# Optimization experiments

Measured on AMD Instinct MI355X. Metric: run time of the kernel, lower is better.

The kernel has to match this reference:

```python
import jax, jax.numpy as jnp
import numpy as np

B, N, C, H = 16, 1029, 1024, 16
D = C // H  # head_dim = 64
N_ROPE = 1024  # patch tokens covered by rope; prefix = N - N_ROPE = 5


def setup_inputs() -> dict:
    key = jax.random.key(0)
    ks = jax.random.split(key, 8)
    x = jax.random.normal(ks[0], (B, N, C), dtype=jnp.float32)
    rope_sin = jax.random.uniform(ks[1], (N_ROPE, D), dtype=jnp.float32, minval=-1.0, maxval=1.0)
    rope_cos = jax.random.uniform(ks[2], (N_ROPE, D), dtype=jnp.float32, minval=-1.0, maxval=1.0)
    s = 1.0 / np.sqrt(C)
    W_qkv = jax.random.normal(ks[3], (3 * C, C), dtype=jnp.float32) * s
    b_qkv = jax.random.normal(ks[4], (3 * C,), dtype=jnp.float32) * 0.02
    W_proj = jax.random.normal(ks[5], (C, C), dtype=jnp.float32) * s
    b_proj = jax.random.normal(ks[6], (C,), dtype=jnp.float32) * 0.02
    return {"x": x, "rope_sin": rope_sin, "rope_cos": rope_cos,
            "W_qkv": W_qkv, "b_qkv": b_qkv, "W_proj": W_proj, "b_proj": b_proj}


def _rotate_half(t):
    t1, t2 = jnp.split(t, 2, axis=-1)
    return jnp.concatenate([-t2, t1], axis=-1)


def _rope_apply(t, sin, cos):
    # t: [B, H, N_rope, D]; sin/cos: [N_rope, D] broadcast over B, H
    return t * cos + _rotate_half(t) * sin


def reference(x, rope_sin, rope_cos, W_qkv, b_qkv, W_proj, b_proj):
    b, n, c = x.shape
    h, d = H, c // H
    # QKV projection (torch Linear: x @ W.T + b)
    qkv = x @ W_qkv.T + b_qkv                       # [B, N, 3C]
    qkv = qkv.reshape(b, n, 3, h, d)
    q = jnp.transpose(qkv[:, :, 0], (0, 2, 1, 3))   # [B, H, N, D]
    k = jnp.transpose(qkv[:, :, 1], (0, 2, 1, 3))
    v = jnp.transpose(qkv[:, :, 2], (0, 2, 1, 3))
    # RoPE on the patch-token suffix only
    prefix = n - rope_sin.shape[-2]
    q = jnp.concatenate([q[:, :, :prefix], _rope_apply(q[:, :, prefix:], rope_sin, rope_cos)], axis=2)
    k = jnp.concatenate([k[:, :, :prefix], _rope_apply(k[:, :, prefix:], rope_sin, rope_cos)], axis=2)
    # Scaled dot-product attention (default scale = 1/sqrt(D))
    scale = 1.0 / jnp.sqrt(jnp.asarray(d, dtype=x.dtype))
    scores = jnp.einsum('bhqd,bhkd->bhqk', q, k) * scale
    attn = jax.nn.softmax(scores, axis=-1)
    out = jnp.einsum('bhqk,bhkd->bhqd', attn, v)    # [B, H, N, D]
    out = jnp.transpose(out, (0, 2, 1, 3)).reshape(b, n, c)
    # Output projection
    return out @ W_proj.T + b_proj
```

## Files before the change

kernel.cpp:

```cpp
#include <hip/hip_runtime.h>
#include <cfloat>
#include <math.h>

#define B_      16
#define N_TOK   1029
#define C_      1024
#define H_      16
#define D_      64
#define PREFIX  5
#define M_ROWS  (B_ * N_TOK)
#define HEAD_SLAB ((size_t)B_ * H_ * N_TOK * D_)
#define VT_STRIDE 1088

typedef __attribute__((ext_vector_type(8))) short bf16x8;
typedef __attribute__((ext_vector_type(4))) float f32x4;

__device__ __forceinline__ unsigned short f2bf(float f) {
    unsigned u = __float_as_uint(f);
    u += 0x7fffu + ((u >> 16) & 1u);
    return (unsigned short)(u >> 16);
}
__device__ __forceinline__ float bf2f(unsigned short h) {
    return __uint_as_float(((unsigned)h) << 16);
}

__global__ __launch_bounds__(256)
void split_kernel(const float* __restrict__ in, unsigned short* __restrict__ hi,
                  unsigned short* __restrict__ lo, int n4)
{
    const int i = blockIdx.x * 256 + threadIdx.x;
    if (i >= n4) return;
    const float4 v = ((const float4*)in)[i];
    ushort4 h, l;
    h.x = f2bf(v.x); l.x = f2bf(v.x - bf2f(h.x));
    h.y = f2bf(v.y); l.y = f2bf(v.y - bf2f(h.y));
    h.z = f2bf(v.z); l.z = f2bf(v.z - bf2f(h.z));
    h.w = f2bf(v.w); l.w = f2bf(v.w - bf2f(h.w));
    ((ushort4*)hi)[i] = h;
    ((ushort4*)lo)[i] = l;
}

__device__ __forceinline__ bf16x8 frag_ld(const unsigned short* slab, int r, int q) {
    const int L = r >> 1;
    const int s = (q | ((r & 1) << 2)) ^ (L & 7);
    return *(const bf16x8*)(slab + L * 64 + s * 8);
}

#define WAIT_BAR(N) do {                                          \
    asm volatile("s_waitcnt vmcnt(" #N ")" ::: "memory");         \
    __builtin_amdgcn_s_barrier();                                 \
    __builtin_amdgcn_sched_barrier(0);                            \
} while (0)

__global__ __launch_bounds__(512, 2)
void gemm_mfma8(const unsigned short* __restrict__ Ahi, const unsigned short* __restrict__ Alo,
                const unsigned short* __restrict__ Whi, const unsigned short* __restrict__ Wlo,
                const float* __restrict__ bias, float* __restrict__ out,
                int M, int Ncols, int K, int scatter)
{
    __shared__ unsigned short lds[2][4][256 * 32];

    const int tid  = threadIdx.x;
    const int wave = tid >> 6;
    const int lane = tid & 63;
    const int lm   = lane & 15;
    const int quad = lane >> 4;
    const int bx = blockIdx.x, by = blockIdx.y;
    const int wm = wave >> 2;
    const int wn = wave & 3;
    const int rowA = by * 256;
    const int rowB = bx * 256;

    f32x4 acc[8][4];
#pragma unroll
    for (int mi = 0; mi < 8; ++mi)
#pragma unroll
        for (int ni = 0; ni < 4; ++ni)
            acc[mi][ni] = (f32x4){0.f, 0.f, 0.f, 0.f};

#define STAGE(buf_, slab_, base_, row0_, doClamp_, k0_) do {                          \
    _Pragma("unroll")                                                                 \
    for (int i_ = 0; i_ < 2; ++i_) {                                                  \
        const int c_ = i_ * 512 + tid;                                                \
        const int L_ = c_ >> 3;                                                       \
        const int u_ = (c_ & 7) ^ (L_ & 7);                                           \
        int grow_ = (row0_) + 2 * L_ + (u_ >> 2);                                     \
        if (doClamp_) grow_ = min(grow_, M - 1);                                      \
        const unsigned short* src_ = (base_) + (size_t)grow_ * K + (k0_) + (u_ & 3) * 8; \
        __builtin_amdgcn_global_load_lds(                                             \
            (__attribute__((address_space(1))) void*)src_,                            \
            (__attribute__((address_space(3))) void*)&lds[buf_][slab_][(i_ * 512 + wave * 64) * 8], \
            16, 0, 0);                                                                \
    }                                                                                 \
} while (0)

    STAGE(0, 0, Ahi, rowA, true,  0);
    STAGE(0, 2, Whi, rowB, false, 0);
    STAGE(0, 3, Wlo, rowB, false, 0);
    STAGE(0, 1, Alo, rowA, true,  0);

    const int NT = K >> 5;
    for (int t = 0; t < NT; ++t) {
        const int cur = t & 1, nxt = cur ^ 1;
        const int tn = (t + 1 == NT) ? 0 : t + 1;
        const int k1 = tn << 5;

        WAIT_BAR(4);
        STAGE(nxt, 0, Ahi, rowA, true,  k1);
        STAGE(nxt, 2, Whi, rowB, false, k1);
        bf16x8 b[4], a[8];
#pragma unroll
        for (int ni = 0; ni < 4; ++ni)
            b[ni] = frag_ld(&lds[cur][2][0], wn * 64 + ni * 16 + lm, quad);
#pragma unroll
        for (int mi = 0; mi < 8; ++mi)
            a[mi] = frag_ld(&lds[cur][0][0], wm * 128 + mi * 16 + lm, quad);
        __builtin_amdgcn_s_setprio(1);
#pragma unroll
        for (int mi = 0; mi < 8; ++mi)
#pragma unroll
            for (int ni = 0; ni < 4; ++ni)
                acc[mi][ni] = __builtin_amdgcn_mfma_f32_16x16x32_bf16(a[mi], b[ni], acc[mi][ni], 0, 0, 0);
        __builtin_amdgcn_s_setprio(0);

        WAIT_BAR(6);
        STAGE(nxt, 3, Wlo, rowB, false, k1);
        __builtin_amdgcn_s_setprio(1);
#pragma unroll
        for (int ni = 0; ni < 4; ++ni) {
            const bf16x8 bl = frag_ld(&lds[cur][3][0], wn * 64 + ni * 16 + lm, quad);
#pragma unroll
            for (int mi = 0; mi < 8; ++mi)
                acc[mi][ni] = __builtin_amdgcn_mfma_f32_16x16x32_bf16(a[mi], bl, acc[mi][ni], 0, 0, 0);
        }
        __builtin_amdgcn_s_setprio(0);

        WAIT_BAR(6);
        STAGE(nxt, 1, Alo, rowA, true, k1);
        __builtin_amdgcn_s_setprio(1);
#pragma unroll
        for (int mi = 0; mi < 8; ++mi) {
            const bf16x8 al = frag_ld(&lds[cur][1][0], wm * 128 + mi * 16 + lm, quad);
#pragma unroll
            for (int ni = 0; ni < 4; ++ni)
                acc[mi][ni] = __builtin_amdgcn_mfma_f32_16x16x32_bf16(al, b[ni], acc[mi][ni], 0, 0, 0);
        }
        __builtin_amdgcn_s_setprio(0);
    }
#undef STAGE
    asm volatile("s_waitcnt vmcnt(0)" ::: "memory");

#pragma unroll
    for (int mi = 0; mi < 8; ++mi) {
#pragma unroll
        for (int rr = 0; rr < 4; ++rr) {
            const int gm = rowA + wm * 128 + mi * 16 + quad * 4 + rr;
            if (gm >= M) continue;
            if (!scatter) {
#pragma unroll
                for (int ni = 0; ni < 4; ++ni) {
                    const int gn = rowB + wn * 64 + ni * 16 + lm;
                    out[(size_t)gm * Ncols + gn] = acc[mi][ni][rr] + bias[gn];
                }
            } else {
                const int b_  = gm / N_TOK;
                const int tok = gm - b_ * N_TOK;
#pragma unroll
                for (int ni = 0; ni < 4; ++ni) {
                    const int gn    = rowB + wn * 64 + ni * 16 + lm;
                    const int which = gn >> 10;
                    const int h     = (gn >> 6) & 15;
                    const int d     = gn & 63;
                    const size_t dst = (size_t)which * HEAD_SLAB +
                                       (((size_t)(b_ * H_ + h)) * N_TOK + tok) * 64 + d;
                    out[dst] = acc[mi][ni][rr] + bias[gn];
                }
            }
        }
    }
}
#undef WAIT_BAR

__global__ __launch_bounds__(256)
void rope_convert(const float* __restrict__ qf, const float* __restrict__ kf,
                  const float* __restrict__ sin_, const float* __restrict__ cos_,
                  unsigned short* __restrict__ qhi, unsigned short* __restrict__ qlo,
                  unsigned short* __restrict__ khi, unsigned short* __restrict__ klo)
{
    const int idx = blockIdx.x * 256 + threadIdx.x;
    const int total = B_ * H_ * N_TOK * 32;
    if (idx >= total) return;
    const int d   = idx & 31;
    const int tmp = idx >> 5;
    const int n   = tmp % N_TOK;
    const int bh  = tmp / N_TOK;

    const size_t base = ((size_t)bh * N_TOK + n) * 64;
    float q1 = qf[base + d], q2 = qf[base + d + 32];
    float k1 = kf[base + d], k2 = kf[base + d + 32];

    if (n >= PREFIX) {
        const int r = n - PREFIX;
        const float c1 = cos_[r * 64 + d];
        const float c2 = cos_[r * 64 + d + 32];
        const float s1 = sin_[r * 64 + d];
        const float s2 = sin_[r * 64 + d + 32];
        const float nq1 = q1 * c1 - q2 * s1;
        const float nq2 = q2 * c2 + q1 * s2;
        q1 = nq1; q2 = nq2;
        const float nk1 = k1 * c1 - k2 * s1;
        const float nk2 = k2 * c2 + k1 * s2;
        k1 = nk1; k2 = nk2;
    }
    q1 *= 0.125f; q2 *= 0.125f;

    unsigned short h;
    h = f2bf(q1); qhi[base + d]      = h; qlo[base + d]      = f2bf(q1 - bf2f(h));
    h = f2bf(q2); qhi[base + d + 32] = h; qlo[base + d + 32] = f2bf(q2 - bf2f(h));
    h = f2bf(k1); khi[base + d]      = h; klo[base + d]      = f2bf(k1 - bf2f(h));
    h = f2bf(k2); khi[base + d + 32] = h; klo[base + d + 32] = f2bf(k2 - bf2f(h));
}

__global__ __launch_bounds__(256)
void v_transpose(const float* __restrict__ vf, unsigned short* __restrict__ vt)
{
    __shared__ float t[64][65];
    const int tid = threadIdx.x;
    const int kt0 = blockIdx.x * 64;
    const int bh  = blockIdx.y;
    const float* src = vf + (size_t)bh * N_TOK * 64;

#pragma unroll
    for (int p = 0; p < 4; ++p) {
        const int e   = p * 256 + tid;
        const int key = e >> 4;
        const int c4  = (e & 15) << 2;
        const int gk  = kt0 + key;
        float4 v = make_float4(0.f, 0.f, 0.f, 0.f);
        if (gk < N_TOK) v = *(const float4*)(src + (size_t)gk * 64 + c4);
        t[key][c4 + 0] = v.x;
        t[key][c4 + 1] = v.y;
        t[key][c4 + 2] = v.z;
        t[key][c4 + 3] = v.w;
    }
    __syncthreads();

    const int d  = tid >> 2;
    const int kb = (tid & 3) << 4;
    unsigned short buf[16];
#pragma unroll
    for (int j = 0; j < 16; ++j) buf[j] = f2bf(t[kb + j][d]);
    unsigned short* dst = vt + (size_t)bh * 64 * VT_STRIDE + (size_t)d * VT_STRIDE + kt0 + kb;
#pragma unroll
    for (int j = 0; j < 4; ++j)
        *(ushort4*)(dst + j * 4) = *(ushort4*)&buf[j * 4];
}

__global__ __launch_bounds__(512, 4)
void attn_mfma2(const unsigned short* __restrict__ qhi_g, const unsigned short* __restrict__ qlo_g,
                const unsigned short* __restrict__ khi_g, const unsigned short* __restrict__ klo_g,
                const unsigned short* __restrict__ vt_g,
                unsigned short* __restrict__ Ohi, unsigned short* __restrict__ Olo)
{
    __shared__ unsigned short Khl[2][64 * 64];
    __shared__ unsigned short Kll[2][64 * 64];
    __shared__ unsigned short Vtl[2][64 * 64];
    __shared__ unsigned short Pl[128 * 64];

    const int tid  = threadIdx.x;
    const int wave = tid >> 6;
    const int lane = tid & 63;
    const int lm   = lane & 15;
    const int quad = lane >> 4;
    const int bh   = blockIdx.x;
    const int q0   = blockIdx.y * 128;
    const int b    = bh >> 4;
    const int h    = bh & 15;

    const unsigned short* Qh  = qhi_g + (size_t)bh * N_TOK * 64;
    const unsigned short* Ql  = qlo_g + (size_t)bh * N_TOK * 64;
    const unsigned short* Khb = khi_g + (size_t)bh * N_TOK * 64;
    const unsigned short* Klb = klo_g + (size_t)bh * N_TOK * 64;
    const unsigned short* Vtb = vt_g  + (size_t)bh * 64 * VT_STRIDE;

#define STAGE(bs, kt0_) do {                                                     \
    const int r_  = tid >> 3;                                                    \
    const int qs_ = tid & 7;                                                     \
    const int sw_ = (qs_ ^ (r_ & 7)) << 3;                                       \
    const int ldsoff_ = wave * 512;                                              \
    const int gk_ = min((kt0_) + r_, N_TOK - 1);                                 \
    __builtin_amdgcn_global_load_lds(                                            \
        (__attribute__((address_space(1))) void*)(Khb + (size_t)gk_ * 64 + sw_), \
        (__attribute__((address_space(3))) void*)&Khl[bs][ldsoff_], 16, 0, 0);   \
    __builtin_amdgcn_global_load_lds(                                            \
        (__attribute__((address_space(1))) void*)(Klb + (size_t)gk_ * 64 + sw_), \
        (__attribute__((address_space(3))) void*)&Kll[bs][ldsoff_], 16, 0, 0);   \
    __builtin_amdgcn_global_load_lds(                                            \
        (__attribute__((address_space(1))) void*)(Vtb + (size_t)r_ * VT_STRIDE + (kt0_) + sw_), \
        (__attribute__((address_space(3))) void*)&Vtl[bs][ldsoff_], 16, 0, 0);   \
} while (0)

    STAGE(0, 0);

    bf16x8 qh[2], ql[2];
    {
        int row = q0 + wave * 16 + lm;
        if (row > N_TOK - 1) row = N_TOK - 1;
#pragma unroll
        for (int s = 0; s < 2; ++s) {
            const size_t off = (size_t)row * 64 + s * 32 + quad * 8;
            qh[s] = *(const bf16x8*)&Qh[off];
            ql[s] = *(const bf16x8*)&Ql[off];
        }
    }

    f32x4 o[4];
    float m_i[4], l_i[4];
#pragma unroll
    for (int r = 0; r < 4; ++r) {
        m_i[r] = -FLT_MAX;
        l_i[r] = 0.f;
        o[r] = (f32x4){0.f, 0.f, 0.f, 0.f};
    }

    asm volatile("s_waitcnt vmcnt(0)\n\ts_barrier" ::: "memory");

    for (int kt = 0; kt < 17; ++kt) {
        const int kt0 = kt * 64;
        const int cur = kt & 1;

        if (kt < 16) STAGE(cur ^ 1, kt0 + 64);

        f32x4 s_acc[4];
#pragma unroll
        for (int ct = 0; ct < 4; ++ct)
            s_acc[ct] = (f32x4){0.f, 0.f, 0.f, 0.f};

#pragma unroll
        for (int ct = 0; ct < 4; ++ct) {
            const int krow = ct * 16 + lm;
#pragma unroll
            for (int s = 0; s < 2; ++s) {
                const int chunk = ((s * 4 + quad) ^ (krow & 7)) << 3;
                const bf16x8 kbh = *(const bf16x8*)&Khl[cur][krow * 64 + chunk];
                const bf16x8 kbl = *(const bf16x8*)&Kll[cur][krow * 64 + chunk];
                s_acc[ct] = __builtin_amdgcn_mfma_f32_16x16x32_bf16(qh[s], kbh, s_acc[ct], 0, 0, 0);
                s_acc[ct] = __builtin_amdgcn_mfma_f32_16x16x32_bf16(qh[s], kbl, s_acc[ct], 0, 0, 0);
                s_acc[ct] = __builtin_amdgcn_mfma_f32_16x16x32_bf16(ql[s], kbh, s_acc[ct], 0, 0, 0);
            }
        }

        if (kt0 + 64 > N_TOK) {
#pragma unroll
            for (int ct = 0; ct < 4; ++ct) {
                if (kt0 + ct * 16 + lm >= N_TOK) {
#pragma unroll
                    for (int r = 0; r < 4; ++r) s_acc[ct][r] = -FLT_MAX;
                }
            }
        }

#pragma unroll
        for (int r = 0; r < 4; ++r) {
            float mt = fmaxf(fmaxf(s_acc[0][r], s_acc[1][r]),
                             fmaxf(s_acc[2][r], s_acc[3][r]));
            mt = fmaxf(mt, __shfl_xor(mt, 1));
            mt = fmaxf(mt, __shfl_xor(mt, 2));
            mt = fmaxf(mt, __shfl_xor(mt, 4));
            mt = fmaxf(mt, __shfl_xor(mt, 8));
            const float mnew  = fmaxf(m_i[r], mt);
            const float alpha = __expf(m_i[r] - mnew);
            float pv[4], rs = 0.f;
#pragma unroll
            for (int ct = 0; ct < 4; ++ct) {
                pv[ct] = __expf(s_acc[ct][r] - mnew);
                rs += pv[ct];
            }
            rs += __shfl_xor(rs, 1);
            rs += __shfl_xor(rs, 2);
            rs += __shfl_xor(rs, 4);
            rs += __shfl_xor(rs, 8);
            l_i[r] = l_i[r] * alpha + rs;
            m_i[r] = mnew;
#pragma unroll
            for (int dt = 0; dt < 4; ++dt) o[dt][r] *= alpha;
            const int prow = wave * 16 + quad * 4 + r;
#pragma unroll
            for (int ct = 0; ct < 4; ++ct) {
                const int col = ct * 16 + lm;
                const int idx = prow * 64 + ((((col >> 3) ^ (prow & 7)) << 3) | (col & 7));
                Pl[idx] = f2bf(pv[ct]);
            }
        }

#pragma unroll
        for (int ks = 0; ks < 2; ++ks) {
            const int prow = wave * 16 + lm;
            const int chunk = ((ks * 4 + quad) ^ (prow & 7)) << 3;
            const bf16x8 pf = *(const bf16x8*)&Pl[prow * 64 + chunk];
#pragma unroll
            for (int dt = 0; dt < 4; ++dt) {
                const int vrow = dt * 16 + lm;
                const int chunkv = ((ks * 4 + quad) ^ (vrow & 7)) << 3;
                const bf16x8 vh = *(const bf16x8*)&Vtl[cur][vrow * 64 + chunkv];
                o[dt] = __builtin_amdgcn_mfma_f32_16x16x32_bf16(pf, vh, o[dt], 0, 0, 0);
            }
        }

        asm volatile("s_waitcnt vmcnt(0)\n\ts_barrier" ::: "memory");
    }
#undef STAGE

#pragma unroll
    for (int r = 0; r < 4; ++r) {
        const int gq = q0 + wave * 16 + quad * 4 + r;
        if (gq >= N_TOK) continue;
        const float inv = 1.0f / l_i[r];
        const size_t base = (((size_t)(b * N_TOK + gq)) * H_ + h) * D_;
#pragma unroll
        for (int dt = 0; dt < 4; ++dt) {
            const float val = o[dt][r] * inv;
            const unsigned short hb = f2bf(val);
            Ohi[base + dt * 16 + lm] = hb;
            Olo[base + dt * 16 + lm] = f2bf(val - bf2f(hb));
        }
    }
}

extern "C" void kernel_launch(void* const* d_in, const int* in_sizes, int n_in,
                              void* d_out, int out_size, void* d_ws, size_t ws_size,
                              hipStream_t stream)
{
    const float* x        = (const float*)d_in[0];
    const float* rope_sin = (const float*)d_in[1];
    const float* rope_cos = (const float*)d_in[2];
    const float* W_qkv    = (const float*)d_in[3];
    const float* b_qkv    = (const float*)d_in[4];
    const float* W_proj   = (const float*)d_in[5];
    const float* b_proj   = (const float*)d_in[6];
    float* out = (float*)d_out;

    float* q_buf = (float*)d_ws;
    float* k_buf = q_buf + HEAD_SLAB;
    float* v_buf = q_buf + 2 * HEAD_SLAB;
    float* slab4 = q_buf + 3 * HEAD_SLAB;

    unsigned short* x_hi = (unsigned short*)slab4;
    unsigned short* x_lo = x_hi + HEAD_SLAB;
    unsigned short* wq_hi = (unsigned short*)d_out;
    unsigned short* wq_lo = wq_hi + (size_t)3 * C_ * C_;

    unsigned short* vthi  = (unsigned short*)d_out;
    unsigned short* qhi   = (unsigned short*)v_buf;
    unsigned short* qlo   = qhi + HEAD_SLAB;
    unsigned short* khi   = (unsigned short*)slab4;
    unsigned short* klo   = khi + HEAD_SLAB;
    unsigned short* attn_hi = (unsigned short*)q_buf;
    unsigned short* attn_lo = attn_hi + HEAD_SLAB;
    unsigned short* wp_hi = (unsigned short*)k_buf;
    unsigned short* wp_lo = wp_hi + (size_t)C_ * C_;

    {
        const int n4x = M_ROWS * C_ / 4;
        split_kernel<<<(n4x + 255) / 256, 256, 0, stream>>>(x, x_hi, x_lo, n4x);
        const int n4q = 3 * C_ * C_ / 4;
        split_kernel<<<(n4q + 255) / 256, 256, 0, stream>>>(W_qkv, wq_hi, wq_lo, n4q);
    }
    {
        dim3 grid(3 * C_ / 256, (M_ROWS + 255) / 256);
        gemm_mfma8<<<grid, 512, 0, stream>>>(x_hi, x_lo, wq_hi, wq_lo, b_qkv,
                                             q_buf, M_ROWS, 3 * C_, C_, 1);
    }
    {
        dim3 grid(17, B_ * H_);
        v_transpose<<<grid, 256, 0, stream>>>(v_buf, vthi);
    }
    {
        const int total = B_ * H_ * N_TOK * 32;
        rope_convert<<<(total + 255) / 256, 256, 0, stream>>>(
            q_buf, k_buf, rope_sin, rope_cos, qhi, qlo, khi, klo);
    }
    {
        dim3 grid(B_ * H_, (N_TOK + 127) / 128);
        attn_mfma2<<<grid, 512, 0, stream>>>(qhi, qlo, khi, klo, vthi,
                                             attn_hi, attn_lo);
    }
    {
        const int n4p = C_ * C_ / 4;
        split_kernel<<<(n4p + 255) / 256, 256, 0, stream>>>(W_proj, wp_hi, wp_lo, n4p);
    }
    {
        dim3 grid(C_ / 256, (M_ROWS + 255) / 256);
        gemm_mfma8<<<grid, 512, 0, stream>>>(attn_hi, attn_lo, wp_hi, wp_lo, b_proj,
                                             out, M_ROWS, C_, C_, 0);
    }
}
```

Baseline: 947.1 us.

## Fuse RoPE and bf16 hi/lo split into QKV GEMM epilogue, drop rope kernel

The QKV GEMM epilogue now applies RoPE, the query scale, and the bf16 hi/lo split directly. It writes bf16 q/k/v slabs instead of fp32 intermediates, which removes the separate rope_convert kernel. v_transpose now reads bf16 V rather than fp32. This cuts global memory round-trips of fp32 Q/K/V. The cost is more epilogue work, register pressure, and sin/cos loads inside the GEMM.

```diff
diff --git a/kernel.cpp b/kernel.cpp
--- a/kernel.cpp
+++ b/kernel.cpp
@@ -56,7 +56,11 @@
 void gemm_mfma8(const unsigned short* __restrict__ Ahi, const unsigned short* __restrict__ Alo,
                 const unsigned short* __restrict__ Whi, const unsigned short* __restrict__ Wlo,
                 const float* __restrict__ bias, float* __restrict__ out,
-                int M, int Ncols, int K, int scatter)
+                int M, int Ncols, int K, int scatter,
+                const float* __restrict__ sinv, const float* __restrict__ cosv,
+                unsigned short* __restrict__ qhi_o, unsigned short* __restrict__ qlo_o,
+                unsigned short* __restrict__ khi_o, unsigned short* __restrict__ klo_o,
+                unsigned short* __restrict__ vhi_o)
 {
     __shared__ unsigned short lds[2][4][256 * 32];
 
@@ -150,30 +154,64 @@
 #undef STAGE
     asm volatile("s_waitcnt vmcnt(0)" ::: "memory");
 
-#pragma unroll
-    for (int mi = 0; mi < 8; ++mi) {
-#pragma unroll
-        for (int rr = 0; rr < 4; ++rr) {
-            const int gm = rowA + wm * 128 + mi * 16 + quad * 4 + rr;
-            if (gm >= M) continue;
-            if (!scatter) {
+    if (!scatter) {
+#pragma unroll
+        for (int mi = 0; mi < 8; ++mi) {
+#pragma unroll
+            for (int rr = 0; rr < 4; ++rr) {
+                const int gm = rowA + wm * 128 + mi * 16 + quad * 4 + rr;
+                if (gm >= M) continue;
 #pragma unroll
                 for (int ni = 0; ni < 4; ++ni) {
                     const int gn = rowB + wn * 64 + ni * 16 + lm;
                     out[(size_t)gm * Ncols + gn] = acc[mi][ni][rr] + bias[gn];
                 }
-            } else {
+            }
+        }
+    } else {
+        const int which = rowB >> 10;
+#pragma unroll
+        for (int mi = 0; mi < 8; ++mi) {
+#pragma unroll
+            for (int rr = 0; rr < 4; ++rr) {
+                const int gm = rowA + wm * 128 + mi * 16 + quad * 4 + rr;
+                if (gm >= M) continue;
                 const int b_  = gm / N_TOK;
                 const int tok = gm - b_ * N_TOK;
-#pragma unroll
-                for (int ni = 0; ni < 4; ++ni) {
-                    const int gn    = rowB + wn * 64 + ni * 16 + lm;
-                    const int which = gn >> 10;
-                    const int h     = (gn >> 6) & 15;
-                    const int d     = gn & 63;
-                    const size_t dst = (size_t)which * HEAD_SLAB +
-                                       (((size_t)(b_ * H_ + h)) * N_TOK + tok) * 64 + d;
-                    out[dst] = acc[mi][ni][rr] + bias[gn];
+                if (which == 2) {
+#pragma unroll
+                    for (int ni = 0; ni < 4; ++ni) {
+                        const int gn = rowB + wn * 64 + ni * 16 + lm;
+                        const int h  = (gn >> 6) & 15;
+                        const int d  = gn & 63;
+                        const float val = acc[mi][ni][rr] + bias[gn];
+                        vhi_o[(((size_t)(b_ * H_ + h)) * N_TOK + tok) * 64 + d] = f2bf(val);
+                    }
+                } else {
+                    unsigned short* hi_ = (which == 0) ? qhi_o : khi_o;
+                    unsigned short* lo_ = (which == 0) ? qlo_o : klo_o;
+                    const float scl = (which == 0) ? 0.125f : 1.0f;
+#pragma unroll
+                    for (int pr = 0; pr < 2; ++pr) {
+                        const int gn1 = rowB + wn * 64 + pr * 16 + lm;
+                        const int h   = (gn1 >> 6) & 15;
+                        const int d1  = gn1 & 63;
+                        float v1 = acc[mi][pr][rr]     + bias[gn1];
+                        float v2 = acc[mi][pr + 2][rr] + bias[gn1 + 32];
+                        if (tok >= PREFIX) {
+                            const int r0 = (tok - PREFIX) * 64 + d1;
+                            const float c1 = cosv[r0],      s1 = sinv[r0];
+                            const float c2 = cosv[r0 + 32], s2 = sinv[r0 + 32];
+                            const float n1 = v1 * c1 - v2 * s1;
+                            const float n2 = v2 * c2 + v1 * s2;
+                            v1 = n1; v2 = n2;
+                        }
+                        v1 *= scl; v2 *= scl;
+                        const size_t base = (((size_t)(b_ * H_ + h)) * N_TOK + tok) * 64 + d1;
+                        unsigned short hb;
+                        hb = f2bf(v1); hi_[base]      = hb; lo_[base]      = f2bf(v1 - bf2f(hb));
+                        hb = f2bf(v2); hi_[base + 32] = hb; lo_[base + 32] = f2bf(v2 - bf2f(hb));
+                    }
                 }
             }
         }
@@ -182,66 +220,27 @@
 #undef WAIT_BAR
 
 __global__ __launch_bounds__(256)
-void rope_convert(const float* __restrict__ qf, const float* __restrict__ kf,
-                  const float* __restrict__ sin_, const float* __restrict__ cos_,
-                  unsigned short* __restrict__ qhi, unsigned short* __restrict__ qlo,
-                  unsigned short* __restrict__ khi, unsigned short* __restrict__ klo)
+void v_transpose(const unsigned short* __restrict__ vf, unsigned short* __restrict__ vt)
 {
-    const int idx = blockIdx.x * 256 + threadIdx.x;
-    const int total = B_ * H_ * N_TOK * 32;
-    if (idx >= total) return;
-    const int d   = idx & 31;
-    const int tmp = idx >> 5;
-    const int n   = tmp % N_TOK;
-    const int bh  = tmp / N_TOK;
-
-    const size_t base = ((size_t)bh * N_TOK + n) * 64;
-    float q1 = qf[base + d], q2 = qf[base + d + 32];
-    float k1 = kf[base + d], k2 = kf[base + d + 32];
-
-    if (n >= PREFIX) {
-        const int r = n - PREFIX;
-        const float c1 = cos_[r * 64 + d];
-        const float c2 = cos_[r * 64 + d + 32];
-        const float s1 = sin_[r * 64 + d];
-        const float s2 = sin_[r * 64 + d + 32];
-        const float nq1 = q1 * c1 - q2 * s1;
-        const float nq2 = q2 * c2 + q1 * s2;
-        q1 = nq1; q2 = nq2;
-        const float nk1 = k1 * c1 - k2 * s1;
-        const float nk2 = k2 * c2 + k1 * s2;
-        k1 = nk1; k2 = nk2;
-    }
-    q1 *= 0.125f; q2 *= 0.125f;
-
-    unsigned short h;
-    h = f2bf(q1); qhi[base + d]      = h; qlo[base + d]      = f2bf(q1 - bf2f(h));
-    h = f2bf(q2); qhi[base + d + 32] = h; qlo[base + d + 32] = f2bf(q2 - bf2f(h));
-    h = f2bf(k1); khi[base + d]      = h; klo[base + d]      = f2bf(k1 - bf2f(h));
-    h = f2bf(k2); khi[base + d + 32] = h; klo[base + d + 32] = f2bf(k2 - bf2f(h));
-}
-
-__global__ __launch_bounds__(256)
-void v_transpose(const float* __restrict__ vf, unsigned short* __restrict__ vt)
-{
-    __shared__ float t[64][65];
+    __shared__ unsigned short t[64][72];
     const int tid = threadIdx.x;
     const int kt0 = blockIdx.x * 64;
     const int bh  = blockIdx.y;
-    const float* src = vf + (size_t)bh * N_TOK * 64;
-
-#pragma unroll
-    for (int p = 0; p < 4; ++p) {
+    const unsigned short* src = vf + (size_t)bh * N_TOK * 64;
+
+#pragma unroll
+    for (int p = 0; p < 2; ++p) {
         const int e   = p * 256 + tid;
-        const int key = e >> 4;
-        const int c4  = (e & 15) << 2;
+        const int key = e >> 3;
+        const int c8  = (e & 7) << 3;
         const int gk  = kt0 + key;
-        float4 v = make_float4(0.f, 0.f, 0.f, 0.f);
-        if (gk < N_TOK) v = *(const float4*)(src + (size_t)gk * 64 + c4);
-        t[key][c4 + 0] = v.x;
-        t[key][c4 + 1] = v.y;
-        t[key][c4 + 2] = v.z;
-        t[key][c4 + 3] = v.w;
+        ushort4 a = make_ushort4(0, 0, 0, 0), b = a;
+        if (gk < N_TOK) {
+            a = *(const ushort4*)(src + (size_t)gk * 64 + c8);
+            b = *(const ushort4*)(src + (size_t)gk * 64 + c8 + 4);
+        }
+        *(ushort4*)&t[key][c8]     = a;
+        *(ushort4*)&t[key][c8 + 4] = b;
     }
     __syncthreads();
 
@@ -249,7 +248,7 @@
     const int kb = (tid & 3) << 4;
     unsigned short buf[16];
 #pragma unroll
-    for (int j = 0; j < 16; ++j) buf[j] = f2bf(t[kb + j][d]);
+    for (int j = 0; j < 16; ++j) buf[j] = t[kb + j][d];
     unsigned short* dst = vt + (size_t)bh * 64 * VT_STRIDE + (size_t)d * VT_STRIDE + kt0 + kb;
 #pragma unroll
     for (int j = 0; j < 4; ++j)
@@ -440,24 +439,26 @@
     const float* b_proj   = (const float*)d_in[6];
     float* out = (float*)d_out;
 
-    float* q_buf = (float*)d_ws;
-    float* k_buf = q_buf + HEAD_SLAB;
-    float* v_buf = q_buf + 2 * HEAD_SLAB;
-    float* slab4 = q_buf + 3 * HEAD_SLAB;
+    float* slab1 = (float*)d_ws;
+    float* slab2 = slab1 + HEAD_SLAB;
+    float* slab3 = slab1 + 2 * HEAD_SLAB;
+    float* slab4 = slab1 + 3 * HEAD_SLAB;
 
     unsigned short* x_hi = (unsigned short*)slab4;
     unsigned short* x_lo = x_hi + HEAD_SLAB;
     unsigned short* wq_hi = (unsigned short*)d_out;
     unsigned short* wq_lo = wq_hi + (size_t)3 * C_ * C_;
 
-    unsigned short* vthi  = (unsigned short*)d_out;
-    unsigned short* qhi   = (unsigned short*)v_buf;
-    unsigned short* qlo   = qhi + HEAD_SLAB;
-    unsigned short* khi   = (unsigned short*)slab4;
-    unsigned short* klo   = khi + HEAD_SLAB;
-    unsigned short* attn_hi = (unsigned short*)q_buf;
+    unsigned short* qhi = (unsigned short*)slab1;
+    unsigned short* qlo = qhi + HEAD_SLAB;
+    unsigned short* khi = (unsigned short*)slab2;
+    unsigned short* klo = khi + HEAD_SLAB;
+    unsigned short* vhi = (unsigned short*)slab3;
+
+    unsigned short* vthi = (unsigned short*)d_out;
+    unsigned short* attn_hi = (unsigned short*)slab4;
     unsigned short* attn_lo = attn_hi + HEAD_SLAB;
-    unsigned short* wp_hi = (unsigned short*)k_buf;
+    unsigned short* wp_hi = (unsigned short*)slab2;
     unsigned short* wp_lo = wp_hi + (size_t)C_ * C_;
 
     {
@@ -469,16 +470,13 @@
     {
         dim3 grid(3 * C_ / 256, (M_ROWS + 255) / 256);
         gemm_mfma8<<<grid, 512, 0, stream>>>(x_hi, x_lo, wq_hi, wq_lo, b_qkv,
-                                             q_buf, M_ROWS, 3 * C_, C_, 1);
+                                             out, M_ROWS, 3 * C_, C_, 1,
+                                             rope_sin, rope_cos,
+                                             qhi, qlo, khi, klo, vhi);
     }
     {
         dim3 grid(17, B_ * H_);
-        v_transpose<<<grid, 256, 0, stream>>>(v_buf, vthi);
-    }
-    {
-        const int total = B_ * H_ * N_TOK * 32;
-        rope_convert<<<(total + 255) / 256, 256, 0, stream>>>(
-            q_buf, k_buf, rope_sin, rope_cos, qhi, qlo, khi, klo);
+        v_transpose<<<grid, 256, 0, stream>>>(vhi, vthi);
     }
     {
         dim3 grid(B_ * H_, (N_TOK + 127) / 128);
@@ -492,6 +490,8 @@
     {
         dim3 grid(C_ / 256, (M_ROWS + 255) / 256);
         gemm_mfma8<<<grid, 512, 0, stream>>>(attn_hi, attn_lo, wp_hi, wp_lo, b_proj,
-                                             out, M_ROWS, C_, C_, 0);
-    }
-}
+                                             out, M_ROWS, C_, C_, 0,
+                                             nullptr, nullptr,
+                                             nullptr, nullptr, nullptr, nullptr, nullptr);
+    }
+}
```

New measurement: 886.3 us. 6.4% less time.
